# Kernel optimization log

Hardware: AMD Instinct MI355X
Metric: run time of the kernel (lower is better)

The kernel has to match this reference:

```python
import jax, jax.numpy as jnp
import numpy as np

N_NODES = 50000


def gcn_conv(x, src, dst, W, b, n_nodes):
    # PyG GCNConv: add self-loops, symmetric normalization D^-1/2 (A+I) D^-1/2 (x W) + b
    E = src.shape[0]
    deg = jax.ops.segment_sum(jnp.ones((E,), x.dtype), dst, num_segments=n_nodes) + 1.0
    dinv = jax.lax.rsqrt(deg)
    h = x @ W  # [N, H]
    norm = dinv[src] * dinv[dst]  # [E]
    agg = jax.ops.segment_sum(h[src] * norm[:, None], dst, num_segments=n_nodes)
    agg = agg + h * (dinv * dinv)[:, None]  # self-loop contribution
    return agg + b


def setup_inputs() -> dict:
    key = jax.random.key(0)
    ks = jax.random.split(key, 16)
    N, E, D, H, T, O = N_NODES, 800000, 128, 128, 2, 1
    x = jax.random.normal(ks[0], (N, D), jnp.float32)
    edge_index = jax.random.randint(ks[1], (2, E), 0, N, jnp.int32)
    edge_attrs = jax.random.uniform(ks[2], (T, E, 7), jnp.float32)
    s = lambda k, sh: jax.random.normal(k, sh, jnp.float32) * (1.0 / np.sqrt(sh[0]))
    return {
        "x": x, "edge_index": edge_index, "edge_attrs": edge_attrs,
        "W1": s(ks[3], (D, H)), "b1": jnp.zeros((H,), jnp.float32),
        "W2": s(ks[4], (H, H)), "b2": jnp.zeros((H,), jnp.float32),
        "W3": s(ks[5], (H, H)), "b3": jnp.zeros((H,), jnp.float32),
        "We": s(ks[6], (2 * H + 7, H)), "be": jnp.zeros((H,), jnp.float32),
        "Wg": s(ks[7], (H, O)), "bg": jnp.zeros((O,), jnp.float32),
    }


def reference(x, edge_index, edge_attrs, W1, b1, W2, b2, W3, b3, We, be, Wg, bg):
    src, dst = edge_index[0], edge_index[1]
    n = x.shape[0]
    outputs = []
    for t in range(edge_attrs.shape[0]):  # small fixed T, x evolves across iterations
        edge_attr = edge_attrs[t]
        x = jax.nn.relu(gcn_conv(x, src, dst, W1, b1, n))
        x = jax.nn.relu(gcn_conv(x, src, dst, W2, b2, n))
        x = jax.nn.relu(gcn_conv(x, src, dst, W3, b3, n))
        # gather-concat-MLP-mean per edge
        edge_features = jnp.concatenate([x[src], x[dst], edge_attr], axis=1)
        edge_output = jax.nn.relu(edge_features @ We + be)
        graph_features = jnp.mean(edge_output, axis=0, keepdims=True)  # [1, H]
        outputs.append(graph_features @ Wg + bg)
        W1 = W2  # no-op placeholder removed below
        W1 = W1  # keep W1 unchanged
    return jnp.concatenate(outputs, axis=0)  # [T, output_dim]
```

## Files before the change

### kernel.cpp

```cpp
#include <hip/hip_runtime.h>
#include <hip/hip_bf16.h>


typedef __attribute__((ext_vector_type(8))) short bf16x8;
typedef __attribute__((ext_vector_type(4))) float f32x4;
typedef __attribute__((ext_vector_type(2))) float f32x2;

__device__ __forceinline__ unsigned short f2bf(float f) {
    union { float f; unsigned int u; } v; v.f = f;
    unsigned int r = v.u + 0x7fffu + ((v.u >> 16) & 1u);
    return (unsigned short)(r >> 16);
}
__device__ __forceinline__ unsigned int pk2bf(float lo, float hi) {
    return (unsigned int)f2bf(lo) | ((unsigned int)f2bf(hi) << 16);
}
__device__ __forceinline__ unsigned char f2fp8(float f) {
    return (unsigned char)(__builtin_amdgcn_cvt_pk_fp8_f32(f, f, 0, false) & 0xff);
}
__device__ __forceinline__ f32x2 max0_2(f32x2 v) {
#if __has_builtin(__builtin_elementwise_max)
    return __builtin_elementwise_max(v, (f32x2){0.f, 0.f});
#else
    return (f32x2){fmaxf(v[0], 0.f), fmaxf(v[1], 0.f)};
#endif
}

__global__ void to_bf16(const float* __restrict__ in, unsigned short* __restrict__ out, int n4)
{
    int i = blockIdx.x * 256 + threadIdx.x;
    if (i < n4) {
        float4 v = ((const float4*)in)[i];
        ushort4 o;
        o.x = f2bf(v.x); o.y = f2bf(v.y); o.z = f2bf(v.z); o.w = f2bf(v.w);
        ((ushort4*)out)[i] = o;
    }
}

__global__ void transpose_w(
    const float* __restrict__ W1, const float* __restrict__ W2,
    const float* __restrict__ W3, const float* __restrict__ We,
    unsigned short* __restrict__ T1, unsigned short* __restrict__ T2,
    unsigned short* __restrict__ T3, unsigned short* __restrict__ Tuv)
{
    const float* src; unsigned short* dst;
    switch (blockIdx.y) {
        case 0:  src = W1;             dst = T1;               break;
        case 1:  src = W2;             dst = T2;               break;
        case 2:  src = W3;             dst = T3;               break;
        case 3:  src = We;             dst = Tuv;              break;
        case 4:  src = We + 128 * 128; dst = Tuv + 128 * 128;  break;
        default: src = W2;             dst = Tuv + 256 * 128;  break;
    }
    for (int i = blockIdx.x * 256 + threadIdx.x; i < 128 * 128; i += 256 * gridDim.x) {
        int k = i >> 7, c = i & 127;
        dst[c * 128 + k] = f2bf(src[i]);
    }
}

__global__ __launch_bounds__(256) void mfma_matmul(
    const unsigned short* __restrict__ X, const unsigned short* __restrict__ Wt,
    unsigned char* __restrict__ out, const float* __restrict__ scale, int n_rows)
{
    const int wave = threadIdx.x >> 6;
    const int lane = threadIdx.x & 63;
    const int m = lane & 15;
    const int q = lane >> 4;
    const int r = blockIdx.x * 64 + wave * 16 + m;
    const bool rv = r < n_rows;

    f32x4 acc[8];
    #pragma unroll
    for (int i = 0; i < 8; ++i) acc[i] = (f32x4){0.f, 0.f, 0.f, 0.f};

    #pragma unroll
    for (int k0 = 0; k0 < 128; k0 += 32) {
        bf16x8 a = {};
        if (rv) a = *(const bf16x8*)(X + (size_t)r * 128 + k0 + q * 8);
        #pragma unroll
        for (int ct = 0; ct < 8; ++ct) {
            bf16x8 b = *(const bf16x8*)(Wt + (ct * 16 + m) * 128 + k0 + q * 8);
            acc[ct] = __builtin_amdgcn_mfma_f32_16x16x32_bf16(a, b, acc[ct], 0, 0, 0);
        }
    }

    #pragma unroll
    for (int reg = 0; reg < 4; ++reg) {
        int gr = blockIdx.x * 64 + wave * 16 + q * 4 + reg;
        if (gr >= n_rows) continue;
        float s = scale[gr];
        #pragma unroll
        for (int ct = 0; ct < 8; ++ct)
            out[(size_t)gr * 128 + ct * 16 + m] = f2fp8(acc[ct][reg] * s);
    }
}

#define FPAD 136
#define GN 16
#define ICAP 64
#define ISTR 72
#define FUSED_LDS (GN * FPAD * 2 + GN * ISTR * 4)
#define EDGE_LDS  10240
#define EM_CHUNK 256

__device__ __forceinline__ void fused_body(
    int bx, char* smem,
    const unsigned char* __restrict__ hs_in, const int* __restrict__ csr_src,
    const int* __restrict__ offs, const int* __restrict__ counts,
    const float* __restrict__ dinv, const float* __restrict__ bias,
    const unsigned short* __restrict__ Wt, int ncols, int uvcols,
    unsigned char* __restrict__ buv, unsigned char* __restrict__ bh, int n)
{
    unsigned short* xs = (unsigned short*)smem;
    int* idxl = (int*)(smem + GN * FPAD * 2);
    const int tid = threadIdx.x;
    const int row = tid >> 4;
    const int node = bx * GN + row;
    const int lg = tid & 15;
    const int c8 = lg * 8;

    if (node < n) {
        const int off = offs[node];
        const int cnt = counts[node];
        const int cap = min(cnt, ICAP);

        for (int j = lg; j < cap; j += 16)
            idxl[row * ISTR + j] = csr_src[off + j];

        const uint2 sv = *(const uint2*)(hs_in + (size_t)node * 128 + c8);

        f32x2 a01 = {0.f, 0.f}, a23 = {0.f, 0.f}, a45 = {0.f, 0.f}, a67 = {0.f, 0.f};
        auto de8 = [&](uint2 v) {
            a01 += __builtin_amdgcn_cvt_pk_f32_fp8(v.x, false);
            a23 += __builtin_amdgcn_cvt_pk_f32_fp8(v.x, true);
            a45 += __builtin_amdgcn_cvt_pk_f32_fp8(v.y, false);
            a67 += __builtin_amdgcn_cvt_pk_f32_fp8(v.y, true);
        };
        uint2 A[4], B[4];
        auto LQ = [&](uint2* Q, int jb) {
            #pragma unroll
            for (int q = 0; q < 4; ++q)
                Q[q] = *(const uint2*)(hs_in + (size_t)idxl[row * ISTR + jb + q] * 128 + c8);
        };
        auto CONS = [&](uint2* Q) {
            #pragma unroll
            for (int q = 0; q < 4; ++q) de8(Q[q]);
        };

        int j = 0;
        if (cap >= 8) {
            LQ(A, 0); LQ(B, 4);
            de8(sv);
            j = 8;
            for (; j + 8 <= cap; j += 8) {
                CONS(A); LQ(A, j);
                CONS(B); LQ(B, j + 4);
            }
            CONS(A); CONS(B);
        } else if (cap >= 4) {
            LQ(A, 0);
            de8(sv);
            CONS(A);
            j = 4;
        } else {
            de8(sv);
        }
        if (j + 4 <= cap) {
            LQ(A, j); CONS(A); j += 4;
        }
        for (; j < cap; ++j)
            de8(*(const uint2*)(hs_in + (size_t)idxl[row * ISTR + j] * 128 + c8));
        for (; j < cnt; ++j)
            de8(*(const uint2*)(hs_in + (size_t)csr_src[off + j] * 128 + c8));

        const float dn = dinv[node];
        const float4 b0 = *(const float4*)(bias + c8);
        const float4 b1v = *(const float4*)(bias + c8 + 4);
        float r0 = fmaxf(fmaf(a01[0], dn, b0.x), 0.f);
        float r1 = fmaxf(fmaf(a01[1], dn, b0.y), 0.f);
        float r2 = fmaxf(fmaf(a23[0], dn, b0.z), 0.f);
        float r3 = fmaxf(fmaf(a23[1], dn, b0.w), 0.f);
        float r4 = fmaxf(fmaf(a45[0], dn, b1v.x), 0.f);
        float r5 = fmaxf(fmaf(a45[1], dn, b1v.y), 0.f);
        float r6 = fmaxf(fmaf(a67[0], dn, b1v.z), 0.f);
        float r7 = fmaxf(fmaf(a67[1], dn, b1v.w), 0.f);
        uint4 w;
        w.x = pk2bf(r0, r1); w.y = pk2bf(r2, r3);
        w.z = pk2bf(r4, r5); w.w = pk2bf(r6, r7);
        *(uint4*)&xs[row * FPAD + c8] = w;
    }
    __syncthreads();

    const int wave = tid >> 6;
    const int lane = tid & 63;
    const int m = lane & 15;
    const int q = lane >> 4;
    const int nct = ncols >> 4;
    const int per = nct >> 2;
    const int ct0 = wave * per;

    for (int ci = 0; ci < per; ++ci) {
        const int ct = ct0 + ci;
        f32x4 acc = (f32x4){0.f, 0.f, 0.f, 0.f};
        #pragma unroll
        for (int k0 = 0; k0 < 128; k0 += 32) {
            bf16x8 a = *(const bf16x8*)&xs[m * FPAD + k0 + q * 8];
            bf16x8 b = *(const bf16x8*)(Wt + (size_t)(ct * 16 + m) * 128 + k0 + q * 8);
            acc = __builtin_amdgcn_mfma_f32_16x16x32_bf16(a, b, acc, 0, 0, 0);
        }
        const int col = ct * 16 + m;
        #pragma unroll
        for (int reg = 0; reg < 4; ++reg) {
            int nd = bx * GN + q * 4 + reg;
            if (nd >= n) continue;
            if (col < uvcols)
                buv[(size_t)nd * 256 + col] = f2fp8(acc[reg]);
            else
                bh[(size_t)nd * 128 + col - uvcols] = f2fp8(acc[reg] * dinv[nd]);
        }
    }
}

__device__ __forceinline__ void edge_body(
    int bx, int nbx, char* smem,
    const unsigned char* __restrict__ uv, const int* __restrict__ src,
    const int* __restrict__ dst, const float* __restrict__ ea,
    const float* __restrict__ We_e, const float* __restrict__ be,
    const float* __restrict__ Wg, float* __restrict__ acc, int E)
{
    float* eas = (float*)smem;
    int*   ss  = (int*)(smem + 7168);
    int*   ds  = (int*)(smem + 8192);
    float* red = (float*)(smem + 9216);

    const int tid  = threadIdx.x;
    const int lane = tid & 31;
    const int g    = tid >> 5;
    const int c4   = lane * 4;

    f32x2 wlo[7], whi[7];
    #pragma unroll
    for (int i = 0; i < 7; ++i) {
        float4 wv = *(const float4*)(We_e + i * 128 + c4);
        wlo[i] = (f32x2){wv.x, wv.y};
        whi[i] = (f32x2){wv.z, wv.w};
    }
    const float4 bev = *(const float4*)(be + c4);
    const f32x2 be01 = (f32x2){bev.x, bev.y};
    const f32x2 be23 = (f32x2){bev.z, bev.w};
    const float4 wg4 = *(const float4*)(Wg + c4);

    f32x2 part01 = {0.f, 0.f}, part23 = {0.f, 0.f};

    for (int base = bx * EM_CHUNK; base < E; base += nbx * EM_CHUNK) {
        const int nch = min(EM_CHUNK, E - base);
        for (int i = tid; i < nch * 7; i += 256)
            eas[i] = ea[(size_t)base * 7 + i];
        for (int i = tid; i < nch; i += 256) {
            ss[i] = src[base + i];
            ds[i] = dst[base + i];
        }
        __syncthreads();

        auto ev = [&](int j) {
            unsigned int us = *(const unsigned int*)(uv + (size_t)ss[j] * 256 + c4);
            unsigned int vs = *(const unsigned int*)(uv + (size_t)ds[j] * 256 + 128 + c4);
            f32x2 u01 = __builtin_amdgcn_cvt_pk_f32_fp8(us, false);
            f32x2 u23 = __builtin_amdgcn_cvt_pk_f32_fp8(us, true);
            f32x2 v01 = __builtin_amdgcn_cvt_pk_f32_fp8(vs, false);
            f32x2 v23 = __builtin_amdgcn_cvt_pk_f32_fp8(vs, true);
            f32x2 val01 = u01 + v01 + be01;
            f32x2 val23 = u23 + v23 + be23;
            const float* eav = &eas[j * 7];
            #pragma unroll
            for (int i = 0; i < 7; ++i) {
                f32x2 e2 = (f32x2){eav[i], eav[i]};
                val01 += e2 * wlo[i];
                val23 += e2 * whi[i];
            }
            part01 += max0_2(val01);
            part23 += max0_2(val23);
        };

        int j = g;
        for (; j + 32 <= nch; j += 32) {
            ev(j); ev(j + 8); ev(j + 16); ev(j + 24);
        }
        for (; j < nch; j += 8)
            ev(j);
        __syncthreads();
    }

    float p = part01[0] * wg4.x + part01[1] * wg4.y + part23[0] * wg4.z + part23[1] * wg4.w;
    red[tid] = p;
    __syncthreads();
    for (int s = 128; s > 0; s >>= 1) {
        if (tid < s) red[tid] += red[tid + s];
        __syncthreads();
    }
    if (tid == 0) atomicAdd(acc, red[0]);
}

__global__ __launch_bounds__(256, 8) void fused_gm(
    const unsigned char* __restrict__ hs_in, const int* __restrict__ csr_src,
    const int* __restrict__ offs, const int* __restrict__ counts,
    const float* __restrict__ dinv, const float* __restrict__ bias,
    const unsigned short* __restrict__ Wt, int ncols, int uvcols,
    unsigned char* __restrict__ buv, unsigned char* __restrict__ bh, int n)
{
    __shared__ __align__(16) char smem[FUSED_LDS];
    fused_body(blockIdx.x, smem, hs_in, csr_src, offs, counts, dinv, bias,
               Wt, ncols, uvcols, buv, bh, n);
}

__global__ __launch_bounds__(256) void edge_mlp(
    const unsigned char* __restrict__ uv, const int* __restrict__ src,
    const int* __restrict__ dst, const float* __restrict__ ea,
    const float* __restrict__ We_e, const float* __restrict__ be,
    const float* __restrict__ Wg, float* __restrict__ acc, int E)
{
    __shared__ __align__(16) char smem[EDGE_LDS];
    edge_body(blockIdx.x, gridDim.x, smem, uv, src, dst, ea, We_e, be, Wg, acc, E);
}

__global__ __launch_bounds__(256, 8) void fused_gm_edge(
    int nf,
    const unsigned char* __restrict__ hs_in, const int* __restrict__ csr_src,
    const int* __restrict__ offs, const int* __restrict__ counts,
    const float* __restrict__ dinv, const float* __restrict__ bias,
    const unsigned short* __restrict__ Wt, int ncols, int uvcols,
    unsigned char* __restrict__ buv, unsigned char* __restrict__ bh, int n,
    int ne,
    const unsigned char* __restrict__ uv, const int* __restrict__ src,
    const int* __restrict__ dst, const float* __restrict__ ea,
    const float* __restrict__ We_e, const float* __restrict__ be,
    const float* __restrict__ Wg, float* __restrict__ acc, int E)
{
    __shared__ __align__(16) char smem[EDGE_LDS];
    const int bid = blockIdx.x;
    const int nmin = (nf < ne) ? nf : ne;
    const int nch8 = nmin >> 3;
    const int inter = nch8 * 16;
    int role, idx;
    if (bid < inter) {
        int gg = bid >> 4, s = bid & 15;
        role = s >> 3;
        idx = gg * 8 + (s & 7);
    } else {
        int r = bid - inter;
        int fleft = nf - nch8 * 8;
        if (r < fleft) { role = 0; idx = nch8 * 8 + r; }
        else           { role = 1; idx = nch8 * 8 + (r - fleft); }
    }
    if (role == 0)
        fused_body(idx, smem, hs_in, csr_src, offs, counts, dinv, bias,
                   Wt, ncols, uvcols, buv, bh, n);
    else
        edge_body(idx, ne, smem, uv, src, dst, ea, We_e, be, Wg, acc, E);
}

__global__ void count_edges(const int* __restrict__ dst, int* __restrict__ counts,
                            int* __restrict__ rank, int E)
{
    int e = blockIdx.x * 256 + threadIdx.x;
    if (e < E) rank[e] = atomicAdd(&counts[dst[e]], 1);
}

__global__ void compute_dinv(const int* __restrict__ counts, float* __restrict__ dinv, int n)
{
    int i = blockIdx.x * 256 + threadIdx.x;
    if (i < n) dinv[i] = rsqrtf((float)counts[i] + 1.0f);
}

__global__ void scan1(const int* __restrict__ counts, int* __restrict__ scanned,
                      int* __restrict__ btot, int n)
{
    __shared__ int sh[256];
    int i = blockIdx.x * 256 + threadIdx.x;
    int v = (i < n) ? counts[i] : 0;
    sh[threadIdx.x] = v;
    __syncthreads();
    for (int off = 1; off < 256; off <<= 1) {
        int t = (threadIdx.x >= off) ? sh[threadIdx.x - off] : 0;
        __syncthreads();
        sh[threadIdx.x] += t;
        __syncthreads();
    }
    if (i < n) scanned[i] = sh[threadIdx.x] - v;
    if (threadIdx.x == 255) btot[blockIdx.x] = sh[255];
}

__global__ void scan2(int* __restrict__ btot, int nb)
{
    __shared__ int sh[256];
    int v = (threadIdx.x < nb) ? btot[threadIdx.x] : 0;
    sh[threadIdx.x] = v;
    __syncthreads();
    for (int off = 1; off < 256; off <<= 1) {
        int t = (threadIdx.x >= off) ? sh[threadIdx.x - off] : 0;
        __syncthreads();
        sh[threadIdx.x] += t;
        __syncthreads();
    }
    if (threadIdx.x < nb) btot[threadIdx.x] = sh[threadIdx.x] - v;
}

__global__ void scan3(const int* __restrict__ scanned, const int* __restrict__ btot,
                      int* __restrict__ offs, int n)
{
    int i = blockIdx.x * 256 + threadIdx.x;
    if (i < n) offs[i] = scanned[i] + btot[blockIdx.x];
}

__global__ void fill_csr2(const int* __restrict__ src, const int* __restrict__ dst,
                          const int* __restrict__ rank, const int* __restrict__ offs,
                          int* __restrict__ csr_src, int E, int n)
{
    const int g8 = blockIdx.x & 7;
    const int b8 = blockIdx.x >> 3;
    const int nb8 = gridDim.x >> 3;
    const int chunk = (n + 7) >> 3;
    const int lo = g8 * chunk;
    const int hi = min(n, lo + chunk);
    for (int e = b8 * 256 + threadIdx.x; e < E; e += nb8 * 256) {
        int d = dst[e];
        if (d >= lo && d < hi)
            csr_src[offs[d] + rank[e]] = src[e];
    }
}

__global__ void write_out(const float* __restrict__ acc, const float* __restrict__ bg,
                          float* __restrict__ out, float invE, int T)
{
    int t = threadIdx.x;
    if (t < T) out[t] = acc[t] * invE + bg[0];
}


extern "C" void kernel_launch(void* const* d_in, const int* in_sizes, int n_in,
                              void* d_out, int out_size, void* d_ws, size_t ws_size,
                              hipStream_t stream)
{
    const float* x   = (const float*)d_in[0];
    const int*  eidx = (const int*)d_in[1];
    const float* ea  = (const float*)d_in[2];
    const float* W1  = (const float*)d_in[3];
    const float* b1  = (const float*)d_in[4];
    const float* W2  = (const float*)d_in[5];
    const float* b2  = (const float*)d_in[6];
    const float* W3  = (const float*)d_in[7];
    const float* b3  = (const float*)d_in[8];
    const float* We  = (const float*)d_in[9];
    const float* be  = (const float*)d_in[10];
    const float* Wg  = (const float*)d_in[11];
    const float* bg  = (const float*)d_in[12];

    const int N = in_sizes[0] / 128;
    const int E = in_sizes[1] / 2;
    const int T = in_sizes[2] / (E * 7);
    const int* src = eidx;
    const int* dst = eidx + E;

    char* wsp = (char*)d_ws;
    auto alloc = [&](size_t bytes) -> char* {
        char* p = wsp;
        wsp += (bytes + 255) / 256 * 256;
        return p;
    };
    int*   counts  = (int*)alloc((size_t)N * 4);
    int*   offs    = (int*)alloc((size_t)N * 4);
    int*   scanned = (int*)alloc((size_t)N * 4);
    int*   btot    = (int*)alloc(1024);
    int*   rank    = (int*)alloc((size_t)E * 4);
    int*   csr_src = (int*)alloc((size_t)E * 4);
    float* dinv    = (float*)alloc((size_t)N * 4);
    float* acc     = (float*)alloc(256);
    unsigned short* X0  = (unsigned short*)alloc((size_t)N * 128 * 2);
    unsigned char*  Bh0 = (unsigned char*)alloc((size_t)N * 128);
    unsigned char*  Bh1 = (unsigned char*)alloc((size_t)N * 128);
    unsigned char*  Buv = (unsigned char*)alloc((size_t)N * 256);
    unsigned short* T1  = (unsigned short*)alloc(128 * 128 * 2);
    unsigned short* T2  = (unsigned short*)alloc(128 * 128 * 2);
    unsigned short* T3  = (unsigned short*)alloc(128 * 128 * 2);
    unsigned short* Tuv = (unsigned short*)alloc(384 * 128 * 2);

    hipMemsetAsync(counts, 0, (size_t)N * 4, stream);
    hipMemsetAsync(acc, 0, (size_t)T * 4, stream);

    to_bf16<<<(N * 128 / 4 + 255) / 256, 256, 0, stream>>>(x, X0, N * 128 / 4);
    transpose_w<<<dim3(8, 6), 256, 0, stream>>>(W1, W2, W3, We, T1, T2, T3, Tuv);

    count_edges<<<(E + 255) / 256, 256, 0, stream>>>(dst, counts, rank, E);
    compute_dinv<<<(N + 255) / 256, 256, 0, stream>>>(counts, dinv, N);
    const int nb = (N + 255) / 256;
    scan1<<<nb, 256, 0, stream>>>(counts, scanned, btot, N);
    scan2<<<1, 256, 0, stream>>>(btot, nb);
    scan3<<<nb, 256, 0, stream>>>(scanned, btot, offs, N);
    fill_csr2<<<2048, 256, 0, stream>>>(src, dst, rank, offs, csr_src, E, N);

    const int mmb = (N + 63) / 64;
    const int fgb = (N + GN - 1) / GN;
    const int emb = (E + EM_CHUNK - 1) / EM_CHUNK;

    unsigned char* hcur = Bh0;
    unsigned char* hnxt = Bh1;
    auto swap = [&]() { unsigned char* tmp = hcur; hcur = hnxt; hnxt = tmp; };

    mfma_matmul<<<mmb, 256, 0, stream>>>(X0, T1, hcur, dinv, N);
    fused_gm<<<fgb, 256, 0, stream>>>(hcur, csr_src, offs, counts, dinv, b1,
                                      T2, 128, 0, Buv, hnxt, N);
    swap();
    fused_gm<<<fgb, 256, 0, stream>>>(hcur, csr_src, offs, counts, dinv, b2,
                                      T3, 128, 0, Buv, hnxt, N);
    swap();

    for (int t = 0; t < T; ++t) {
        const bool last = (t == T - 1);
        fused_gm<<<fgb, 256, 0, stream>>>(hcur, csr_src, offs, counts, dinv, b3,
                                          Tuv, last ? 256 : 384, 256, Buv, hnxt, N);
        if (last) {
            edge_mlp<<<emb, 256, 0, stream>>>(Buv, src, dst, ea + (size_t)t * E * 7,
                                              We + 256 * 128, be, Wg, acc + t, E);
        } else {
            swap();
            fused_gm_edge<<<fgb + emb, 256, 0, stream>>>(
                fgb, hcur, csr_src, offs, counts, dinv, b1, T2, 128, 0, Buv, hnxt, N,
                emb, Buv, src, dst, ea + (size_t)t * E * 7,
                We + 256 * 128, be, Wg, acc + t, E);
            swap();
            fused_gm<<<fgb, 256, 0, stream>>>(hcur, csr_src, offs, counts, dinv, b2,
                                              T3, 128, 0, Buv, hnxt, N);
            swap();
        }
    }
    write_out<<<1, 64, 0, stream>>>(acc, bg, (float*)d_out, 1.0f / (float)E, T);
}
```

Baseline: 542.0 us.

## Widen blocks to 512 threads and split edge MLP across two fused GCN launches

Fused GCN gather kernels now use 512 threads, with 32 lanes per node each handling 4 features instead of 16 lanes handling 8, and 8 waves share the MFMA column tiles. The edge MLP now processes one 512-edge chunk per block instead of grid-striding. Its work is split in half and co-scheduled with the next two GCN layer launches instead of one, to balance work and overlap the edge pass. The degree normalisation computation is folded into the scan kernel to drop a launch. The narrower per-lane gathers and larger blocks may change memory-level parallelism and occupancy.

```diff
diff --git a/kernel.cpp b/kernel.cpp
--- a/kernel.cpp
+++ b/kernel.cpp
@@ -99,8 +99,8 @@
 #define ICAP 64
 #define ISTR 72
 #define FUSED_LDS (GN * FPAD * 2 + GN * ISTR * 4)
-#define EDGE_LDS  10240
-#define EM_CHUNK 256
+#define EM_CHUNK 512
+#define EDGE_LDS (EM_CHUNK * 7 * 4 + EM_CHUNK * 4 * 2 + 512 * 4)
 
 __device__ __forceinline__ void fused_body(
     int bx, char* smem,
@@ -113,43 +113,41 @@
     unsigned short* xs = (unsigned short*)smem;
     int* idxl = (int*)(smem + GN * FPAD * 2);
     const int tid = threadIdx.x;
-    const int row = tid >> 4;
+    const int row = tid >> 5;
     const int node = bx * GN + row;
-    const int lg = tid & 15;
-    const int c8 = lg * 8;
+    const int lg = tid & 31;
+    const int c4 = lg * 4;
 
     if (node < n) {
         const int off = offs[node];
         const int cnt = counts[node];
         const int cap = min(cnt, ICAP);
 
-        for (int j = lg; j < cap; j += 16)
+        for (int j = lg; j < cap; j += 32)
             idxl[row * ISTR + j] = csr_src[off + j];
 
-        const uint2 sv = *(const uint2*)(hs_in + (size_t)node * 128 + c8);
-
-        f32x2 a01 = {0.f, 0.f}, a23 = {0.f, 0.f}, a45 = {0.f, 0.f}, a67 = {0.f, 0.f};
-        auto de8 = [&](uint2 v) {
-            a01 += __builtin_amdgcn_cvt_pk_f32_fp8(v.x, false);
-            a23 += __builtin_amdgcn_cvt_pk_f32_fp8(v.x, true);
-            a45 += __builtin_amdgcn_cvt_pk_f32_fp8(v.y, false);
-            a67 += __builtin_amdgcn_cvt_pk_f32_fp8(v.y, true);
+        const unsigned int sv = *(const unsigned int*)(hs_in + (size_t)node * 128 + c4);
+
+        f32x2 a01 = {0.f, 0.f}, a23 = {0.f, 0.f};
+        auto de4 = [&](unsigned int v) {
+            a01 += __builtin_amdgcn_cvt_pk_f32_fp8(v, false);
+            a23 += __builtin_amdgcn_cvt_pk_f32_fp8(v, true);
         };
-        uint2 A[4], B[4];
-        auto LQ = [&](uint2* Q, int jb) {
+        unsigned int A[4], B[4];
+        auto LQ = [&](unsigned int* Q, int jb) {
             #pragma unroll
             for (int q = 0; q < 4; ++q)
-                Q[q] = *(const uint2*)(hs_in + (size_t)idxl[row * ISTR + jb + q] * 128 + c8);
+                Q[q] = *(const unsigned int*)(hs_in + (size_t)idxl[row * ISTR + jb + q] * 128 + c4);
         };
-        auto CONS = [&](uint2* Q) {
+        auto CONS = [&](unsigned int* Q) {
             #pragma unroll
-            for (int q = 0; q < 4; ++q) de8(Q[q]);
+            for (int q = 0; q < 4; ++q) de4(Q[q]);
         };
 
         int j = 0;
         if (cap >= 8) {
             LQ(A, 0); LQ(B, 4);
-            de8(sv);
+            de4(sv);
             j = 8;
             for (; j + 8 <= cap; j += 8) {
                 CONS(A); LQ(A, j);
@@ -158,35 +156,29 @@
             CONS(A); CONS(B);
         } else if (cap >= 4) {
             LQ(A, 0);
-            de8(sv);
+            de4(sv);
             CONS(A);
             j = 4;
         } else {
-            de8(sv);
+            de4(sv);
         }
         if (j + 4 <= cap) {
             LQ(A, j); CONS(A); j += 4;
         }
         for (; j < cap; ++j)
-            de8(*(const uint2*)(hs_in + (size_t)idxl[row * ISTR + j] * 128 + c8));
+            de4(*(const unsigned int*)(hs_in + (size_t)idxl[row * ISTR + j] * 128 + c4));
         for (; j < cnt; ++j)
-            de8(*(const uint2*)(hs_in + (size_t)csr_src[off + j] * 128 + c8));
+            de4(*(const unsigned int*)(hs_in + (size_t)csr_src[off + j] * 128 + c4));
 
         const float dn = dinv[node];
-        const float4 b0 = *(const float4*)(bias + c8);
-        const float4 b1v = *(const float4*)(bias + c8 + 4);
-        float r0 = fmaxf(fmaf(a01[0], dn, b0.x), 0.f);
-        float r1 = fmaxf(fmaf(a01[1], dn, b0.y), 0.f);
-        float r2 = fmaxf(fmaf(a23[0], dn, b0.z), 0.f);
-        float r3 = fmaxf(fmaf(a23[1], dn, b0.w), 0.f);
-        float r4 = fmaxf(fmaf(a45[0], dn, b1v.x), 0.f);
-        float r5 = fmaxf(fmaf(a45[1], dn, b1v.y), 0.f);
-        float r6 = fmaxf(fmaf(a67[0], dn, b1v.z), 0.f);
-        float r7 = fmaxf(fmaf(a67[1], dn, b1v.w), 0.f);
-        uint4 w;
+        const float4 bb = *(const float4*)(bias + c4);
+        float r0 = fmaxf(fmaf(a01[0], dn, bb.x), 0.f);
+        float r1 = fmaxf(fmaf(a01[1], dn, bb.y), 0.f);
+        float r2 = fmaxf(fmaf(a23[0], dn, bb.z), 0.f);
+        float r3 = fmaxf(fmaf(a23[1], dn, bb.w), 0.f);
+        uint2 w;
         w.x = pk2bf(r0, r1); w.y = pk2bf(r2, r3);
-        w.z = pk2bf(r4, r5); w.w = pk2bf(r6, r7);
-        *(uint4*)&xs[row * FPAD + c8] = w;
+        *(uint2*)&xs[row * FPAD + c4] = w;
     }
     __syncthreads();
 
@@ -195,7 +187,7 @@
     const int m = lane & 15;
     const int q = lane >> 4;
     const int nct = ncols >> 4;
-    const int per = nct >> 2;
+    const int per = nct >> 3;
     const int ct0 = wave * per;
 
     for (int ci = 0; ci < per; ++ci) {
@@ -221,16 +213,16 @@
 }
 
 __device__ __forceinline__ void edge_body(
-    int bx, int nbx, char* smem,
+    int chunk, char* smem,
     const unsigned char* __restrict__ uv, const int* __restrict__ src,
     const int* __restrict__ dst, const float* __restrict__ ea,
     const float* __restrict__ We_e, const float* __restrict__ be,
     const float* __restrict__ Wg, float* __restrict__ acc, int E)
 {
     float* eas = (float*)smem;
-    int*   ss  = (int*)(smem + 7168);
-    int*   ds  = (int*)(smem + 8192);
-    float* red = (float*)(smem + 9216);
+    int*   ss  = (int*)(smem + EM_CHUNK * 7 * 4);
+    int*   ds  = (int*)(smem + EM_CHUNK * 7 * 4 + EM_CHUNK * 4);
+    float* red = (float*)(smem + EM_CHUNK * 7 * 4 + EM_CHUNK * 8);
 
     const int tid  = threadIdx.x;
     const int lane = tid & 31;
@@ -251,56 +243,55 @@
 
     f32x2 part01 = {0.f, 0.f}, part23 = {0.f, 0.f};
 
-    for (int base = bx * EM_CHUNK; base < E; base += nbx * EM_CHUNK) {
-        const int nch = min(EM_CHUNK, E - base);
-        for (int i = tid; i < nch * 7; i += 256)
-            eas[i] = ea[(size_t)base * 7 + i];
-        for (int i = tid; i < nch; i += 256) {
-            ss[i] = src[base + i];
-            ds[i] = dst[base + i];
-        }
-        __syncthreads();
-
-        auto ev = [&](int j) {
-            unsigned int us = *(const unsigned int*)(uv + (size_t)ss[j] * 256 + c4);
-            unsigned int vs = *(const unsigned int*)(uv + (size_t)ds[j] * 256 + 128 + c4);
-            f32x2 u01 = __builtin_amdgcn_cvt_pk_f32_fp8(us, false);
-            f32x2 u23 = __builtin_amdgcn_cvt_pk_f32_fp8(us, true);
-            f32x2 v01 = __builtin_amdgcn_cvt_pk_f32_fp8(vs, false);
-            f32x2 v23 = __builtin_amdgcn_cvt_pk_f32_fp8(vs, true);
-            f32x2 val01 = u01 + v01 + be01;
-            f32x2 val23 = u23 + v23 + be23;
-            const float* eav = &eas[j * 7];
-            #pragma unroll
-            for (int i = 0; i < 7; ++i) {
-                f32x2 e2 = (f32x2){eav[i], eav[i]};
-                val01 += e2 * wlo[i];
-                val23 += e2 * whi[i];
-            }
-            part01 += max0_2(val01);
-            part23 += max0_2(val23);
-        };
-
-        int j = g;
-        for (; j + 32 <= nch; j += 32) {
-            ev(j); ev(j + 8); ev(j + 16); ev(j + 24);
-        }
-        for (; j < nch; j += 8)
-            ev(j);
-        __syncthreads();
-    }
+    const int base = chunk * EM_CHUNK;
+    const int nch = min(EM_CHUNK, E - base);
+    for (int i = tid; i < nch * 7; i += 512)
+        eas[i] = ea[(size_t)base * 7 + i];
+    for (int i = tid; i < nch; i += 512) {
+        ss[i] = src[base + i];
+        ds[i] = dst[base + i];
+    }
+    __syncthreads();
+
+    auto ev = [&](int j) {
+        unsigned int us = *(const unsigned int*)(uv + (size_t)ss[j] * 256 + c4);
+        unsigned int vs = *(const unsigned int*)(uv + (size_t)ds[j] * 256 + 128 + c4);
+        f32x2 u01 = __builtin_amdgcn_cvt_pk_f32_fp8(us, false);
+        f32x2 u23 = __builtin_amdgcn_cvt_pk_f32_fp8(us, true);
+        f32x2 v01 = __builtin_amdgcn_cvt_pk_f32_fp8(vs, false);
+        f32x2 v23 = __builtin_amdgcn_cvt_pk_f32_fp8(vs, true);
+        f32x2 val01 = u01 + v01 + be01;
+        f32x2 val23 = u23 + v23 + be23;
+        const float* eav = &eas[j * 7];
+        #pragma unroll
+        for (int i = 0; i < 7; ++i) {
+            f32x2 e2 = (f32x2){eav[i], eav[i]};
+            val01 += e2 * wlo[i];
+            val23 += e2 * whi[i];
+        }
+        part01 += max0_2(val01);
+        part23 += max0_2(val23);
+    };
+
+    int j = g;
+    for (; j + 64 <= nch; j += 64) {
+        ev(j); ev(j + 16); ev(j + 32); ev(j + 48);
+    }
+    for (; j < nch; j += 16)
+        ev(j);
+    __syncthreads();
 
     float p = part01[0] * wg4.x + part01[1] * wg4.y + part23[0] * wg4.z + part23[1] * wg4.w;
     red[tid] = p;
     __syncthreads();
-    for (int s = 128; s > 0; s >>= 1) {
+    for (int s = 256; s > 0; s >>= 1) {
         if (tid < s) red[tid] += red[tid + s];
         __syncthreads();
     }
     if (tid == 0) atomicAdd(acc, red[0]);
 }
 
-__global__ __launch_bounds__(256, 8) void fused_gm(
+__global__ __launch_bounds__(512, 8) void fused_gm(
     const unsigned char* __restrict__ hs_in, const int* __restrict__ csr_src,
     const int* __restrict__ offs, const int* __restrict__ counts,
     const float* __restrict__ dinv, const float* __restrict__ bias,
@@ -312,24 +303,24 @@
                Wt, ncols, uvcols, buv, bh, n);
 }
 
-__global__ __launch_bounds__(256) void edge_mlp(
+__global__ __launch_bounds__(512, 8) void edge_mlp(
     const unsigned char* __restrict__ uv, const int* __restrict__ src,
     const int* __restrict__ dst, const float* __restrict__ ea,
     const float* __restrict__ We_e, const float* __restrict__ be,
     const float* __restrict__ Wg, float* __restrict__ acc, int E)
 {
     __shared__ __align__(16) char smem[EDGE_LDS];
-    edge_body(blockIdx.x, gridDim.x, smem, uv, src, dst, ea, We_e, be, Wg, acc, E);
-}
-
-__global__ __launch_bounds__(256, 8) void fused_gm_edge(
+    edge_body(blockIdx.x, smem, uv, src, dst, ea, We_e, be, Wg, acc, E);
+}
+
+__global__ __launch_bounds__(512, 8) void fused_gm_edge(
     int nf,
     const unsigned char* __restrict__ hs_in, const int* __restrict__ csr_src,
     const int* __restrict__ offs, const int* __restrict__ counts,
     const float* __restrict__ dinv, const float* __restrict__ bias,
     const unsigned short* __restrict__ Wt, int ncols, int uvcols,
     unsigned char* __restrict__ buv, unsigned char* __restrict__ bh, int n,
-    int ne,
+    int ne, int ec0,
     const unsigned char* __restrict__ uv, const int* __restrict__ src,
     const int* __restrict__ dst, const float* __restrict__ ea,
     const float* __restrict__ We_e, const float* __restrict__ be,
@@ -355,7 +346,7 @@
         fused_body(idx, smem, hs_in, csr_src, offs, counts, dinv, bias,
                    Wt, ncols, uvcols, buv, bh, n);
     else
-        edge_body(idx, ne, smem, uv, src, dst, ea, We_e, be, Wg, acc, E);
+        edge_body(ec0 + idx, smem, uv, src, dst, ea, We_e, be, Wg, acc, E);
 }
 
 __global__ void count_edges(const int* __restrict__ dst, int* __restrict__ counts,
@@ -365,18 +356,13 @@
     if (e < E) rank[e] = atomicAdd(&counts[dst[e]], 1);
 }
 
-__global__ void compute_dinv(const int* __restrict__ counts, float* __restrict__ dinv, int n)
-{
-    int i = blockIdx.x * 256 + threadIdx.x;
-    if (i < n) dinv[i] = rsqrtf((float)counts[i] + 1.0f);
-}
-
 __global__ void scan1(const int* __restrict__ counts, int* __restrict__ scanned,
-                      int* __restrict__ btot, int n)
+                      int* __restrict__ btot, float* __restrict__ dinv, int n)
 {
     __shared__ int sh[256];
     int i = blockIdx.x * 256 + threadIdx.x;
     int v = (i < n) ? counts[i] : 0;
+    if (i < n) dinv[i] = rsqrtf((float)v + 1.0f);
     sh[threadIdx.x] = v;
     __syncthreads();
     for (int off = 1; off < 256; off <<= 1) {
@@ -490,9 +476,8 @@
     transpose_w<<<dim3(8, 6), 256, 0, stream>>>(W1, W2, W3, We, T1, T2, T3, Tuv);
 
     count_edges<<<(E + 255) / 256, 256, 0, stream>>>(dst, counts, rank, E);
-    compute_dinv<<<(N + 255) / 256, 256, 0, stream>>>(counts, dinv, N);
     const int nb = (N + 255) / 256;
-    scan1<<<nb, 256, 0, stream>>>(counts, scanned, btot, N);
+    scan1<<<nb, 256, 0, stream>>>(counts, scanned, btot, dinv, N);
     scan2<<<1, 256, 0, stream>>>(btot, nb);
     scan3<<<nb, 256, 0, stream>>>(scanned, btot, offs, N);
     fill_csr2<<<2048, 256, 0, stream>>>(src, dst, rank, offs, csr_src, E, N);
@@ -500,35 +485,39 @@
     const int mmb = (N + 63) / 64;
     const int fgb = (N + GN - 1) / GN;
     const int emb = (E + EM_CHUNK - 1) / EM_CHUNK;
+    const int eh0 = (emb + 1) / 2;
+    const int eh1 = emb - eh0;
 
     unsigned char* hcur = Bh0;
     unsigned char* hnxt = Bh1;
     auto swap = [&]() { unsigned char* tmp = hcur; hcur = hnxt; hnxt = tmp; };
 
     mfma_matmul<<<mmb, 256, 0, stream>>>(X0, T1, hcur, dinv, N);
-    fused_gm<<<fgb, 256, 0, stream>>>(hcur, csr_src, offs, counts, dinv, b1,
+    fused_gm<<<fgb, 512, 0, stream>>>(hcur, csr_src, offs, counts, dinv, b1,
                                       T2, 128, 0, Buv, hnxt, N);
     swap();
-    fused_gm<<<fgb, 256, 0, stream>>>(hcur, csr_src, offs, counts, dinv, b2,
+    fused_gm<<<fgb, 512, 0, stream>>>(hcur, csr_src, offs, counts, dinv, b2,
                                       T3, 128, 0, Buv, hnxt, N);
     swap();
 
     for (int t = 0; t < T; ++t) {
         const bool last = (t == T - 1);
-        fused_gm<<<fgb, 256, 0, stream>>>(hcur, csr_src, offs, counts, dinv, b3,
+        fused_gm<<<fgb, 512, 0, stream>>>(hcur, csr_src, offs, counts, dinv, b3,
                                           Tuv, last ? 256 : 384, 256, Buv, hnxt, N);
         if (last) {
-            edge_mlp<<<emb, 256, 0, stream>>>(Buv, src, dst, ea + (size_t)t * E * 7,
+            edge_mlp<<<emb, 512, 0, stream>>>(Buv, src, dst, ea + (size_t)t * E * 7,
                                               We + 256 * 128, be, Wg, acc + t, E);
         } else {
             swap();
-            fused_gm_edge<<<fgb + emb, 256, 0, stream>>>(
+            fused_gm_edge<<<fgb + eh0, 512, 0, stream>>>(
                 fgb, hcur, csr_src, offs, counts, dinv, b1, T2, 128, 0, Buv, hnxt, N,
-                emb, Buv, src, dst, ea + (size_t)t * E * 7,
+                eh0, 0, Buv, src, dst, ea + (size_t)t * E * 7,
                 We + 256 * 128, be, Wg, acc + t, E);
             swap();
-            fused_gm<<<fgb, 256, 0, stream>>>(hcur, csr_src, offs, counts, dinv, b2,
-                                              T3, 128, 0, Buv, hnxt, N);
+            fused_gm_edge<<<fgb + eh1, 512, 0, stream>>>(
+                fgb, hcur, csr_src, offs, counts, dinv, b2, T3, 128, 0, Buv, hnxt, N,
+                eh1, eh0, Buv, src, dst, ea + (size_t)t * E * 7,
+                We + 256 * 128, be, Wg, acc + t, E);
             swap();
         }
     }
```

Measured after the change: 563.0 us. +3.9%, slower.
